# Performance work log

Hardware: AMD Instinct MI355X
Metric: run time of the kernel (lower is better)

## Reference

```python
import jax, jax.numpy as jnp
import numpy as np


def setup_inputs() -> dict:
    key = jax.random.key(0)
    k1, k2 = jax.random.split(key)
    B, C_IN, C_OUT, K = 256, 1024, 1024, 16
    curr_input = jax.random.normal(k1, (B, C_IN, K), dtype=jnp.float32)
    weight = jax.random.normal(k2, (C_OUT, C_IN, K), dtype=jnp.float32)
    return {"curr_input": curr_input, "weight": weight}


def reference(curr_input, weight):
    # Steady-state streaming conv step:
    # output[b, o] = sum_{c,k} curr_input[b, c, k] * weight[o, c, k]
    # This is exactly the triple nested torch.dot loop, fused into one contraction.
    return jnp.einsum("bck,ock->bo", curr_input, weight)
```

## Files before the change

### kernel.cpp

```cpp
#include <hip/hip_runtime.h>
#include <hip/hip_bf16.h>


#define CO    1024
#define KTOT  16384
#define BM    256
#define BN    128
#define NB    8
#define SKB   32
#define KC    (KTOT / SKB)
#define BK    32
#define KITERS (KC / BK)
#define SLICE_ELEMS (BM * CO)

typedef __attribute__((ext_vector_type(8))) short short8;
typedef __attribute__((ext_vector_type(4))) float f32x4;
typedef __attribute__((ext_vector_type(4))) unsigned short u16x4;

__device__ __forceinline__ unsigned short f2bf(float f) {
    union { __bf16 h; unsigned short u; } c; c.h = (__bf16)f; return c.u;
}

__device__ __forceinline__ void gl_lds16(const float* g, const float* lds_uniform) {
    __builtin_amdgcn_global_load_lds(
        (const __attribute__((address_space(1))) void*)g,
        (__attribute__((address_space(3))) void*)lds_uniform, 16, 0, 0);
}

template <bool USE_WS>
__global__ __launch_bounds__(512, 2)
void sconv_gemm_v6(const float* __restrict__ A, const float* __restrict__ W,
                   float* __restrict__ out, unsigned short* __restrict__ wsb) {
    __shared__ float lA[2][BM * BK];
    __shared__ float lB[2][BN * BK];

    const int tid  = threadIdx.x;
    const int wid  = tid >> 6;
    const int lane = tid & 63;

    const int wgid = blockIdx.x;
    const int c  = wgid & 7;
    const int rs = wgid >> 3;
    const int nb = rs & 7;
    const int kb = (rs >> 3) * 8 + c;
    const int bn = nb * BN;
    const int k0 = kb * KC;

    const float* Asrc = A + k0;
    const float* Wsrc = W + (size_t)bn * KTOT + k0;

    int aRow[4], aGk[4], aLds[4];
    #pragma unroll
    for (int j = 0; j < 4; ++j) {
        int s = j * 512 + tid;
        aRow[j] = s >> 3;
        aGk[j]  = (s & 7) ^ (aRow[j] & 7);
        aLds[j] = (j * 512 + wid * 64) * 4;
    }
    int bRow[2], bGk[2], bLds[2];
    #pragma unroll
    for (int j = 0; j < 2; ++j) {
        int s = j * 512 + tid;
        bRow[j] = s >> 3;
        bGk[j]  = (s & 7) ^ (bRow[j] & 7);
        bLds[j] = (j * 512 + wid * 64) * 4;
    }

#define STAGE(BUF, T) {                                                          \
        _Pragma("unroll")                                                        \
        for (int j = 0; j < 4; ++j)                                              \
            gl_lds16(Asrc + (size_t)aRow[j] * KTOT + (T) * BK + aGk[j] * 4,      \
                     &lA[BUF][aLds[j]]);                                         \
        _Pragma("unroll")                                                        \
        for (int j = 0; j < 2; ++j)                                              \
            gl_lds16(Wsrc + (size_t)bRow[j] * KTOT + (T) * BK + bGk[j] * 4,      \
                     &lB[BUF][bLds[j]]);                                         \
    }

    const int wm = (wid >> 1) * 64;
    const int wn = (wid & 1) * 64;
    const int q  = lane >> 4;
    const int fr = lane & 15;

    f32x4 acc[4][4] = {};

#define COMPUTE(BUF) {                                                           \
        short8 bf[4];                                                            \
        _Pragma("unroll")                                                        \
        for (int ni = 0; ni < 4; ++ni) {                                         \
            int r = wn + ni * 16 + fr;                                           \
            int sw = r & 7;                                                      \
            f32x4 v0 = *(const f32x4*)&lB[BUF][r * BK + (((q*2)     ^ sw) * 4)]; \
            f32x4 v1 = *(const f32x4*)&lB[BUF][r * BK + (((q*2 + 1) ^ sw) * 4)]; \
            short8 tb;                                                           \
            tb[0]=f2bf(v0[0]); tb[1]=f2bf(v0[1]); tb[2]=f2bf(v0[2]); tb[3]=f2bf(v0[3]); \
            tb[4]=f2bf(v1[0]); tb[5]=f2bf(v1[1]); tb[6]=f2bf(v1[2]); tb[7]=f2bf(v1[3]); \
            bf[ni] = tb;                                                         \
        }                                                                        \
        _Pragma("unroll")                                                        \
        for (int mi = 0; mi < 4; ++mi) {                                         \
            int r = wm + mi * 16 + fr;                                           \
            int sw = r & 7;                                                      \
            f32x4 v0 = *(const f32x4*)&lA[BUF][r * BK + (((q*2)     ^ sw) * 4)]; \
            f32x4 v1 = *(const f32x4*)&lA[BUF][r * BK + (((q*2 + 1) ^ sw) * 4)]; \
            short8 af;                                                           \
            af[0]=f2bf(v0[0]); af[1]=f2bf(v0[1]); af[2]=f2bf(v0[2]); af[3]=f2bf(v0[3]); \
            af[4]=f2bf(v1[0]); af[5]=f2bf(v1[1]); af[6]=f2bf(v1[2]); af[7]=f2bf(v1[3]); \
            _Pragma("unroll")                                                    \
            for (int ni = 0; ni < 4; ++ni)                                       \
                acc[mi][ni] = __builtin_amdgcn_mfma_f32_16x16x32_bf16(           \
                    af, bf[ni], acc[mi][ni], 0, 0, 0);                           \
        }                                                                        \
    }

    STAGE(0, 0);
    #pragma unroll
    for (int t = 0; t < KITERS; ++t) {
        const int buf = t & 1;
        asm volatile("" ::: "memory");
        __builtin_amdgcn_s_barrier();
        asm volatile("" ::: "memory");
        if (t + 1 < KITERS) {
            STAGE(buf ^ 1, t + 1);
            asm volatile("s_waitcnt vmcnt(6)" ::: "memory");
        } else {
            asm volatile("s_waitcnt vmcnt(0)" ::: "memory");
        }
        __builtin_amdgcn_s_barrier();
        asm volatile("" ::: "memory");
        COMPUTE(buf);
    }
#undef STAGE
#undef COMPUTE

    if (USE_WS) {
        unsigned short* slice = wsb + (size_t)kb * SLICE_ELEMS;
        const int pbase = bn + wn + fr * 4;
        #pragma unroll
        for (int mi = 0; mi < 4; ++mi) {
            #pragma unroll
            for (int j = 0; j < 4; ++j) {
                const int r = wm + mi * 16 + q * 4 + j;
                u16x4 v;
                #pragma unroll
                for (int ni = 0; ni < 4; ++ni) v[ni] = f2bf(acc[mi][ni][j]);
                *(u16x4*)&slice[(size_t)r * CO + pbase] = v;
            }
        }
    } else {
        #pragma unroll
        for (int mi = 0; mi < 4; ++mi)
            #pragma unroll
            for (int ni = 0; ni < 4; ++ni) {
                const int col = bn + wn + ni * 16 + fr;
                #pragma unroll
                for (int j = 0; j < 4; ++j) {
                    const int r = wm + mi * 16 + q * 4 + j;
                    unsafeAtomicAdd(out + (size_t)r * CO + col, acc[mi][ni][j]);
                }
            }
    }
}

__global__ __launch_bounds__(256)
void reduce_splitk_v6(const unsigned short* __restrict__ ws, float* __restrict__ out) {
    const int g = blockIdx.x * 256 + threadIdx.x;
    const u16x4* base = (const u16x4*)ws;
    float s[4] = {0, 0, 0, 0};
    #pragma unroll 8
    for (int sdx = 0; sdx < SKB; ++sdx) {
        u16x4 v = base[(size_t)sdx * (SLICE_ELEMS / 4) + g];
        #pragma unroll
        for (int e = 0; e < 4; ++e) {
            unsigned int u = ((unsigned int)v[e]) << 16;
            s[e] += __builtin_bit_cast(float, u);
        }
    }
    const int r   = g >> 8;
    const int p   = g & 255;
    const int c64 = p >> 4;
    const int L   = p & 15;
    float* orow = out + (size_t)r * CO + c64 * 64 + L;
    #pragma unroll
    for (int e = 0; e < 4; ++e) orow[e * 16] = s[e];
}

extern "C" void kernel_launch(void* const* d_in, const int* in_sizes, int n_in,
                              void* d_out, int out_size, void* d_ws, size_t ws_size,
                              hipStream_t stream) {
    const float* A = (const float*)d_in[0];
    const float* W = (const float*)d_in[1];
    float* out = (float*)d_out;
    unsigned short* ws = (unsigned short*)d_ws;

    const size_t ws_needed = (size_t)SKB * SLICE_ELEMS * sizeof(unsigned short);

    if (ws_size >= ws_needed) {
        sconv_gemm_v6<true><<<NB * SKB, 512, 0, stream>>>(A, W, out, ws);
        reduce_splitk_v6<<<SLICE_ELEMS / 4 / 256, 256, 0, stream>>>(ws, out);
    } else {
        hipMemsetAsync(d_out, 0, (size_t)out_size * sizeof(float), stream);
        sconv_gemm_v6<false><<<NB * SKB, 512, 0, stream>>>(A, W, out, ws);
    }
}
```

Measured before the change: 29.66 us.

## Convert tiles to bf16 at staging, double split-K, raise occupancy

Staging now goes through registers instead of direct global-to-LDS loads. Each tile is converted to bf16 once and stored in padded bf16 LDS tiles, so the compute loop reads short8 fragments with no per-fragment conversion. This halves LDS footprint, which allows four workgroups per CU, and split-K is doubled to 64 slices so more workgroups run. The costs are that global loads are no longer overlapped asynchronously with the LDS write, and the workspace and reduction traffic double.

```diff
diff --git a/kernel.cpp b/kernel.cpp
--- a/kernel.cpp
+++ b/kernel.cpp
@@ -7,10 +7,11 @@
 #define BM    256
 #define BN    128
 #define NB    8
-#define SKB   32
+#define SKB   64
 #define KC    (KTOT / SKB)
 #define BK    32
 #define KITERS (KC / BK)
+#define LDA   40
 #define SLICE_ELEMS (BM * CO)
 
 typedef __attribute__((ext_vector_type(8))) short short8;
@@ -21,18 +22,21 @@
     union { __bf16 h; unsigned short u; } c; c.h = (__bf16)f; return c.u;
 }
 
-__device__ __forceinline__ void gl_lds16(const float* g, const float* lds_uniform) {
-    __builtin_amdgcn_global_load_lds(
-        (const __attribute__((address_space(1))) void*)g,
-        (__attribute__((address_space(3))) void*)lds_uniform, 16, 0, 0);
+__device__ __forceinline__ short8 pack8(f32x4 a, f32x4 b) {
+    short8 r;
+    r[0] = (short)f2bf(a[0]); r[1] = (short)f2bf(a[1]);
+    r[2] = (short)f2bf(a[2]); r[3] = (short)f2bf(a[3]);
+    r[4] = (short)f2bf(b[0]); r[5] = (short)f2bf(b[1]);
+    r[6] = (short)f2bf(b[2]); r[7] = (short)f2bf(b[3]);
+    return r;
 }
 
 template <bool USE_WS>
-__global__ __launch_bounds__(512, 2)
-void sconv_gemm_v6(const float* __restrict__ A, const float* __restrict__ W,
+__global__ __launch_bounds__(512, 4)
+void sconv_gemm_v8(const float* __restrict__ A, const float* __restrict__ W,
                    float* __restrict__ out, unsigned short* __restrict__ wsb) {
-    __shared__ float lA[2][BM * BK];
-    __shared__ float lB[2][BN * BK];
+    __shared__ __align__(16) unsigned short lA[2][BM * LDA];
+    __shared__ __align__(16) unsigned short lB[2][BN * LDA];
 
     const int tid  = threadIdx.x;
     const int wid  = tid >> 6;
@@ -46,35 +50,25 @@
     const int bn = nb * BN;
     const int k0 = kb * KC;
 
-    const float* Asrc = A + k0;
-    const float* Wsrc = W + (size_t)bn * KTOT + k0;
+    const int aR = tid >> 2, aG = tid & 3;
+    const int bR = tid >> 2, bG = tid & 3;
+    const float* Ap0 = A + (size_t)aR * KTOT + k0 + aG * 8;
+    const float* Ap1 = Ap0 + (size_t)128 * KTOT;
+    const float* Bp  = W + (size_t)(bn + bR) * KTOT + k0 + bG * 8;
+    const int wA0 = aR * LDA + aG * 8;
+    const int wA1 = wA0 + 128 * LDA;
+    const int wB  = bR * LDA + bG * 8;
 
-    int aRow[4], aGk[4], aLds[4];
-    #pragma unroll
-    for (int j = 0; j < 4; ++j) {
-        int s = j * 512 + tid;
-        aRow[j] = s >> 3;
-        aGk[j]  = (s & 7) ^ (aRow[j] & 7);
-        aLds[j] = (j * 512 + wid * 64) * 4;
-    }
-    int bRow[2], bGk[2], bLds[2];
-    #pragma unroll
-    for (int j = 0; j < 2; ++j) {
-        int s = j * 512 + tid;
-        bRow[j] = s >> 3;
-        bGk[j]  = (s & 7) ^ (bRow[j] & 7);
-        bLds[j] = (j * 512 + wid * 64) * 4;
-    }
-
-#define STAGE(BUF, T) {                                                          \
-        _Pragma("unroll")                                                        \
-        for (int j = 0; j < 4; ++j)                                              \
-            gl_lds16(Asrc + (size_t)aRow[j] * KTOT + (T) * BK + aGk[j] * 4,      \
-                     &lA[BUF][aLds[j]]);                                         \
-        _Pragma("unroll")                                                        \
-        for (int j = 0; j < 2; ++j)                                              \
-            gl_lds16(Wsrc + (size_t)bRow[j] * KTOT + (T) * BK + bGk[j] * 4,      \
-                     &lB[BUF][bLds[j]]);                                         \
+#define STAGE(BUF, T) {                                                       \
+        f32x4 a00 = *(const f32x4*)(Ap0 + (T) * BK);                          \
+        f32x4 a01 = *(const f32x4*)(Ap0 + (T) * BK + 4);                      \
+        f32x4 a10 = *(const f32x4*)(Ap1 + (T) * BK);                          \
+        f32x4 a11 = *(const f32x4*)(Ap1 + (T) * BK + 4);                      \
+        f32x4 b0  = *(const f32x4*)(Bp  + (T) * BK);                          \
+        f32x4 b1  = *(const f32x4*)(Bp  + (T) * BK + 4);                      \
+        *(short8*)&lA[BUF][wA0] = pack8(a00, a01);                            \
+        *(short8*)&lA[BUF][wA1] = pack8(a10, a11);                            \
+        *(short8*)&lB[BUF][wB]  = pack8(b0, b1);                              \
     }
 
     const int wm = (wid >> 1) * 64;
@@ -82,53 +76,36 @@
     const int q  = lane >> 4;
     const int fr = lane & 15;
 
+    int offA[4], offB[4];
+    #pragma unroll
+    for (int mi = 0; mi < 4; ++mi) offA[mi] = (wm + mi * 16 + fr) * LDA + q * 8;
+    #pragma unroll
+    for (int ni = 0; ni < 4; ++ni) offB[ni] = (wn + ni * 16 + fr) * LDA + q * 8;
+
     f32x4 acc[4][4] = {};
 
-#define COMPUTE(BUF) {                                                           \
-        short8 bf[4];                                                            \
-        _Pragma("unroll")                                                        \
-        for (int ni = 0; ni < 4; ++ni) {                                         \
-            int r = wn + ni * 16 + fr;                                           \
-            int sw = r & 7;                                                      \
-            f32x4 v0 = *(const f32x4*)&lB[BUF][r * BK + (((q*2)     ^ sw) * 4)]; \
-            f32x4 v1 = *(const f32x4*)&lB[BUF][r * BK + (((q*2 + 1) ^ sw) * 4)]; \
-            short8 tb;                                                           \
-            tb[0]=f2bf(v0[0]); tb[1]=f2bf(v0[1]); tb[2]=f2bf(v0[2]); tb[3]=f2bf(v0[3]); \
-            tb[4]=f2bf(v1[0]); tb[5]=f2bf(v1[1]); tb[6]=f2bf(v1[2]); tb[7]=f2bf(v1[3]); \
-            bf[ni] = tb;                                                         \
-        }                                                                        \
-        _Pragma("unroll")                                                        \
-        for (int mi = 0; mi < 4; ++mi) {                                         \
-            int r = wm + mi * 16 + fr;                                           \
-            int sw = r & 7;                                                      \
-            f32x4 v0 = *(const f32x4*)&lA[BUF][r * BK + (((q*2)     ^ sw) * 4)]; \
-            f32x4 v1 = *(const f32x4*)&lA[BUF][r * BK + (((q*2 + 1) ^ sw) * 4)]; \
-            short8 af;                                                           \
-            af[0]=f2bf(v0[0]); af[1]=f2bf(v0[1]); af[2]=f2bf(v0[2]); af[3]=f2bf(v0[3]); \
-            af[4]=f2bf(v1[0]); af[5]=f2bf(v1[1]); af[6]=f2bf(v1[2]); af[7]=f2bf(v1[3]); \
-            _Pragma("unroll")                                                    \
-            for (int ni = 0; ni < 4; ++ni)                                       \
-                acc[mi][ni] = __builtin_amdgcn_mfma_f32_16x16x32_bf16(           \
-                    af, bf[ni], acc[mi][ni], 0, 0, 0);                           \
-        }                                                                        \
+#define COMPUTE(BUF) {                                                        \
+        short8 bf[4];                                                         \
+        _Pragma("unroll")                                                     \
+        for (int ni = 0; ni < 4; ++ni)                                        \
+            bf[ni] = *(const short8*)&lB[BUF][offB[ni]];                      \
+        _Pragma("unroll")                                                     \
+        for (int mi = 0; mi < 4; ++mi) {                                      \
+            short8 af = *(const short8*)&lA[BUF][offA[mi]];                   \
+            _Pragma("unroll")                                                 \
+            for (int ni = 0; ni < 4; ++ni)                                    \
+                acc[mi][ni] = __builtin_amdgcn_mfma_f32_16x16x32_bf16(        \
+                    af, bf[ni], acc[mi][ni], 0, 0, 0);                        \
+        }                                                                     \
     }
 
     STAGE(0, 0);
+    __syncthreads();
     #pragma unroll
     for (int t = 0; t < KITERS; ++t) {
-        const int buf = t & 1;
-        asm volatile("" ::: "memory");
-        __builtin_amdgcn_s_barrier();
-        asm volatile("" ::: "memory");
-        if (t + 1 < KITERS) {
-            STAGE(buf ^ 1, t + 1);
-            asm volatile("s_waitcnt vmcnt(6)" ::: "memory");
-        } else {
-            asm volatile("s_waitcnt vmcnt(0)" ::: "memory");
-        }
-        __builtin_amdgcn_s_barrier();
-        asm volatile("" ::: "memory");
-        COMPUTE(buf);
+        COMPUTE(t & 1);
+        if (t + 1 < KITERS) STAGE((t + 1) & 1, t + 1);
+        __syncthreads();
     }
 #undef STAGE
 #undef COMPUTE
@@ -163,7 +140,7 @@
 }
 
 __global__ __launch_bounds__(256)
-void reduce_splitk_v6(const unsigned short* __restrict__ ws, float* __restrict__ out) {
+void reduce_splitk_v8(const unsigned short* __restrict__ ws, float* __restrict__ out) {
     const int g = blockIdx.x * 256 + threadIdx.x;
     const u16x4* base = (const u16x4*)ws;
     float s[4] = {0, 0, 0, 0};
@@ -196,10 +173,10 @@
     const size_t ws_needed = (size_t)SKB * SLICE_ELEMS * sizeof(unsigned short);
 
     if (ws_size >= ws_needed) {
-        sconv_gemm_v6<true><<<NB * SKB, 512, 0, stream>>>(A, W, out, ws);
-        reduce_splitk_v6<<<SLICE_ELEMS / 4 / 256, 256, 0, stream>>>(ws, out);
+        sconv_gemm_v8<true><<<NB * SKB, 512, 0, stream>>>(A, W, out, ws);
+        reduce_splitk_v8<<<SLICE_ELEMS / 4 / 256, 256, 0, stream>>>(ws, out);
     } else {
         hipMemsetAsync(d_out, 0, (size_t)out_size * sizeof(float), stream);
-        sconv_gemm_v6<false><<<NB * SKB, 512, 0, stream>>>(A, W, out, ws);
+        sconv_gemm_v8<false><<<NB * SKB, 512, 0, stream>>>(A, W, out, ws);
     }
 }
```

Result: slower. 30.89 us (+4.2%).
